# Performance work log

Hardware: AMD Instinct MI355X
Metric: run time of the kernel (lower is better)

Reference implementation:

```python
import jax, jax.numpy as jnp
import numpy as np

NEG_SLOPE = 0.2

def _leaky_relu(x):
    return jnp.where(x >= 0, x, NEG_SLOPE * x)

def setup_inputs() -> dict:
    key = jax.random.key(0)
    ks = jax.random.split(key, 12)
    B, N, M = 64, 4096, 128
    d_ope, d_ma, d_out = 6, 3, 8
    return {
        "ope_ma_adj": jax.random.randint(ks[0], (B, N, M), 0, 2, dtype=jnp.int32),
        "batch_idxes": jnp.arange(B, dtype=jnp.int32),
        "ope_feat": jax.random.normal(ks[1], (B, N, d_ope), dtype=jnp.float32),
        "ma_feat": jax.random.normal(ks[2], (B, M, d_ma), dtype=jnp.float32),
        "proc_time": jax.random.uniform(ks[3], (B, N, M), dtype=jnp.float32),
        "W_src": jax.random.normal(ks[4], (d_ope, d_out), dtype=jnp.float32),
        "W_dst": jax.random.normal(ks[5], (d_ma, d_out), dtype=jnp.float32),
        "w_edge": jax.random.normal(ks[6], (d_out,), dtype=jnp.float32),
        "attn_l": jax.random.normal(ks[7], (d_out,), dtype=jnp.float32),
        "attn_r": jax.random.normal(ks[8], (d_out,), dtype=jnp.float32),
        "attn_e": jax.random.normal(ks[9], (d_out,), dtype=jnp.float32),
    }

def reference(ope_ma_adj, batch_idxes, ope_feat, ma_feat, proc_time,
              W_src, W_dst, w_edge, attn_l, attn_r, attn_e):
    # GATedge.forward with num_head=1 (head dim folded away).
    adj_i = ope_ma_adj[batch_idxes]            # [B,N,M] int (0/1)
    adj = adj_i.astype(jnp.float32)
    feat_src = ope_feat @ W_src                # [B,N,d]
    feat_dst = ma_feat @ W_dst                 # [B,M,d]
    el = feat_src @ attn_l                     # [B,N]
    er = feat_dst @ attn_r                     # [B,M]
    # fc_edge is Linear(1,d): feat_edge = proc[...,None]*w_edge, so
    # ee = (feat_edge*attn_e).sum(-1) = proc * dot(w_edge, attn_e)
    ee = proc_time * jnp.dot(w_edge, attn_e)   # [B,N,M]
    a = adj * el[:, :, None] + ee + adj * er[:, None, :]
    eijk = _leaky_relu(a)                      # [B,N,M]
    ekk = _leaky_relu(2.0 * er)                # [B,M]
    neg_inf = jnp.asarray(-jnp.inf, dtype=eijk.dtype)
    eijk_m = jnp.where(adj_i == 1, eijk, neg_inf)
    e = jnp.concatenate([eijk_m, ekk[:, None, :]], axis=1)   # [B,N+1,M]
    alpha = jax.nn.softmax(e, axis=1)          # softmax over ops (+self)
    alpha_ijk = alpha[:, :-1, :]               # [B,N,M]
    alpha_kk = alpha[:, -1, :]                 # [B,M]
    # b = sum_j alpha_ijk * (feat_edge + feat_src), split to avoid [B,N,M,d]
    b_edge = jnp.einsum('bnm,bnm->bm', alpha_ijk, proc_time)[..., None] * w_edge  # [B,M,d]
    b_src = jnp.einsum('bnm,bnd->bmd', alpha_ijk, feat_src)                       # [B,M,d]
    c = feat_dst * alpha_kk[..., None]         # [B,M,d]
    return jax.nn.sigmoid(b_edge + b_src + c)  # nu_k_prime [B,M,d]
```

## Files before the change

kernel.cpp:

```cpp
#include <hip/hip_runtime.h>
#include <hip/hip_bf16.h>

constexpr int B  = 64;
constexpr int N  = 4096;
constexpr int M  = 128;
constexpr int DO = 8;
constexpr int NC = 32;
constexpr int CH = N / NC;
constexpr int RW = CH / 4;
constexpr int NS = RW / 2;
constexpr float CEXP = 20.0f;

constexpr int waitimm(int n) { return (n & 15) | ((n >> 4) << 14) | (7 << 4) | (15 << 8); }

typedef __attribute__((address_space(3))) void       lds_void;
typedef const __attribute__((address_space(1))) void gbl_void;

__global__ __launch_bounds__(256) void hgnn_k1(
    const int*   __restrict__ adj,
    const int*   __restrict__ bidx,
    const float* __restrict__ ope_feat,
    const float* __restrict__ ma_feat,
    const float* __restrict__ proc,
    const float* __restrict__ W_src,
    const float* __restrict__ W_dst,
    const float* __restrict__ w_edge,
    const float* __restrict__ attn_l,
    const float* __restrict__ attn_r,
    const float* __restrict__ attn_e,
    float*       __restrict__ acc)
{
    const int chunk = blockIdx.x;
    const int b     = blockIdx.y;
    const int t     = threadIdx.x;
    const int w     = t >> 6;
    const int lane  = t & 63;
    const int n0    = chunk * CH;

    __shared__ __align__(16) int   bufA[4][4][256];
    __shared__ __align__(16) float bufP[4][4][256];
    __shared__ __align__(16) float fs[CH][DO];
    __shared__ float el_s[CH];

    const int c0 = lane;
    const int c1 = lane + 64;

    float er0 = 0.f, er1 = 0.f, cee = 0.f;
    {
        const float* mf0 = ma_feat + ((size_t)b * M + c0) * 3;
        const float* mf1 = ma_feat + ((size_t)b * M + c1) * 3;
        const float a0 = mf0[0], a1 = mf0[1], a2 = mf0[2];
        const float b0 = mf1[0], b1 = mf1[1], b2 = mf1[2];
#pragma unroll
        for (int d = 0; d < DO; ++d) {
            er0 += (a0 * W_dst[d] + a1 * W_dst[DO + d] + a2 * W_dst[2 * DO + d]) * attn_r[d];
            er1 += (b0 * W_dst[d] + b1 * W_dst[DO + d] + b2 * W_dst[2 * DO + d]) * attn_r[d];
            cee += w_edge[d] * attn_e[d];
        }
    }

    if (t < CH) {
        const float* of = ope_feat + ((size_t)b * N + (n0 + t)) * 6;
        const float o0 = of[0], o1 = of[1], o2 = of[2], o3 = of[3], o4 = of[4], o5 = of[5];
        float el = 0.f;
#pragma unroll
        for (int d = 0; d < DO; ++d) {
            const float f = o0 * W_src[d] + o1 * W_src[DO + d] + o2 * W_src[2 * DO + d] +
                            o3 * W_src[3 * DO + d] + o4 * W_src[4 * DO + d] + o5 * W_src[5 * DO + d];
            fs[t][d] = f;
            el += f * attn_l[d];
        }
        el_s[t] = el;
    }
    __syncthreads();

    const int ab = bidx[b];
    const int*   adjw  = adj  + ((size_t)ab * N + n0 + w * RW) * M;
    const float* procw = proc + ((size_t)b  * N + n0 + w * RW) * M;
    const int l4 = lane * 4;

    auto issue = [&](int S) {
        __builtin_amdgcn_global_load_lds((gbl_void*)(adjw + (size_t)S * 256 + l4),
                                         (lds_void*)&bufA[w][S & 3][0], 16, 0, 0);
        __builtin_amdgcn_global_load_lds((gbl_void*)(procw + (size_t)S * 256 + l4),
                                         (lds_void*)&bufP[w][S & 3][0], 16, 0, 0);
    };

    float l0 = 0.f, sp0 = 0.f, l1 = 0.f, sp1 = 0.f;
    float sf0[DO], sf1[DO];
#pragma unroll
    for (int d = 0; d < DO; ++d) { sf0[d] = 0.f; sf1[d] = 0.f; }

    auto consume = [&](int S) {
        const int sb = (S & 3) * 256;
        const int* bA = &bufA[w][0][0];
        const float* bP = &bufP[w][0][0];
#pragma unroll
        for (int rr = 0; rr < 2; ++rr) {
            const int r = w * RW + S * 2 + rr;
            const float  el = el_s[r];
            const float4 f0 = *reinterpret_cast<const float4*>(&fs[r][0]);
            const float4 f1 = *reinterpret_cast<const float4*>(&fs[r][4]);
            const int   a0 = bA[sb + rr * 128 + c0];
            const int   a1 = bA[sb + rr * 128 + c1];
            const float p0 = bP[sb + rr * 128 + c0];
            const float p1 = bP[sb + rr * 128 + c1];
            {
                float v = el + er0 + cee * p0;
                v = (v >= 0.f) ? v : 0.2f * v;
                const float wt = __expf(((a0 != 0) ? v : -1e30f) - CEXP);
                l0 += wt; sp0 = fmaf(wt, p0, sp0);
                sf0[0] = fmaf(wt, f0.x, sf0[0]); sf0[1] = fmaf(wt, f0.y, sf0[1]);
                sf0[2] = fmaf(wt, f0.z, sf0[2]); sf0[3] = fmaf(wt, f0.w, sf0[3]);
                sf0[4] = fmaf(wt, f1.x, sf0[4]); sf0[5] = fmaf(wt, f1.y, sf0[5]);
                sf0[6] = fmaf(wt, f1.z, sf0[6]); sf0[7] = fmaf(wt, f1.w, sf0[7]);
            }
            {
                float v = el + er1 + cee * p1;
                v = (v >= 0.f) ? v : 0.2f * v;
                const float wt = __expf(((a1 != 0) ? v : -1e30f) - CEXP);
                l1 += wt; sp1 = fmaf(wt, p1, sp1);
                sf1[0] = fmaf(wt, f0.x, sf1[0]); sf1[1] = fmaf(wt, f0.y, sf1[1]);
                sf1[2] = fmaf(wt, f0.z, sf1[2]); sf1[3] = fmaf(wt, f0.w, sf1[3]);
                sf1[4] = fmaf(wt, f1.x, sf1[4]); sf1[5] = fmaf(wt, f1.y, sf1[5]);
                sf1[6] = fmaf(wt, f1.z, sf1[6]); sf1[7] = fmaf(wt, f1.w, sf1[7]);
            }
        }
    };

    issue(0); issue(1); issue(2); issue(3);

#define STEP_MI(S) { __builtin_amdgcn_s_waitcnt(waitimm(6)); consume(S); issue((S) + 4); }
#define STEP_NI(S, WN) { __builtin_amdgcn_s_waitcnt(waitimm(WN)); consume(S); }
    STEP_MI(0)  STEP_MI(1)  STEP_MI(2)  STEP_MI(3)
    STEP_MI(4)  STEP_MI(5)  STEP_MI(6)  STEP_MI(7)
    STEP_MI(8)  STEP_MI(9)  STEP_MI(10) STEP_MI(11)
    STEP_NI(12, 6) STEP_NI(13, 4) STEP_NI(14, 2) STEP_NI(15, 0)
#undef STEP_MI
#undef STEP_NI

    float* R = reinterpret_cast<float*>(&bufA[0][0][0]);
    const size_t colbase = (size_t)b * M;

    __syncthreads();
    {
        float v0[5] = {l0, sp0, sf0[0], sf0[1], sf0[2]};
        float v1[5] = {l1, sp1, sf1[0], sf1[1], sf1[2]};
#pragma unroll
        for (int k = 0; k < 5; ++k) {
            R[(w * 5 + k) * 128 + c0] = v0[k];
            R[(w * 5 + k) * 128 + c1] = v1[k];
        }
    }
    __syncthreads();
    if (t < M) {
#pragma unroll
        for (int k = 0; k < 5; ++k) {
            const float s = R[(0 * 5 + k) * 128 + t] + R[(1 * 5 + k) * 128 + t] +
                            R[(2 * 5 + k) * 128 + t] + R[(3 * 5 + k) * 128 + t];
            atomicAdd(&acc[(size_t)k * (B * M) + colbase + t], s);
        }
    }
    __syncthreads();
    {
        float v0[5] = {sf0[3], sf0[4], sf0[5], sf0[6], sf0[7]};
        float v1[5] = {sf1[3], sf1[4], sf1[5], sf1[6], sf1[7]};
#pragma unroll
        for (int k = 0; k < 5; ++k) {
            R[(w * 5 + k) * 128 + c0] = v0[k];
            R[(w * 5 + k) * 128 + c1] = v1[k];
        }
    }
    __syncthreads();
    if (t < M) {
#pragma unroll
        for (int k = 0; k < 5; ++k) {
            const float s = R[(0 * 5 + k) * 128 + t] + R[(1 * 5 + k) * 128 + t] +
                            R[(2 * 5 + k) * 128 + t] + R[(3 * 5 + k) * 128 + t];
            atomicAdd(&acc[(size_t)(5 + k) * (B * M) + colbase + t], s);
        }
    }
}

__global__ __launch_bounds__(256) void hgnn_k2(
    const float* __restrict__ ma_feat,
    const float* __restrict__ W_dst,
    const float* __restrict__ w_edge,
    const float* __restrict__ attn_r,
    const float* __restrict__ acc,
    float*       __restrict__ out)
{
    const int t = blockIdx.x * 256 + threadIdx.x;
    if (t >= B * M) return;
    const int m = t & (M - 1);
    const int b = t >> 7;

    float a[10];
#pragma unroll
    for (int f = 0; f < 10; ++f) a[f] = acc[(size_t)f * (B * M) + t];

    const float* mf = ma_feat + ((size_t)b * M + m) * 3;
    const float f0 = mf[0], f1 = mf[1], f2 = mf[2];
    float fd[DO];
    float er = 0.f;
#pragma unroll
    for (int d = 0; d < DO; ++d) {
        fd[d] = f0 * W_dst[d] + f1 * W_dst[DO + d] + f2 * W_dst[2 * DO + d];
        er += fd[d] * attn_r[d];
    }
    float ekk = 2.f * er;
    ekk = (ekk >= 0.f) ? ekk : 0.2f * ekk;
    const float wkk = __expf(ekk - CEXP);

    const float L    = a[0] + wkk;
    const float invL = 1.f / L;
    const float akk  = wkk * invL;
    const float spf  = a[1] * invL;

#pragma unroll
    for (int d = 0; d < DO; ++d) {
        const float x = spf * w_edge[d] + a[2 + d] * invL + fd[d] * akk;
        out[(size_t)t * DO + d] = 1.f / (1.f + __expf(-x));
    }
}

extern "C" void kernel_launch(void* const* d_in, const int* in_sizes, int n_in,
                              void* d_out, int out_size, void* d_ws, size_t ws_size,
                              hipStream_t stream) {
    const int*   adj      = (const int*)  d_in[0];
    const int*   bidx     = (const int*)  d_in[1];
    const float* ope_feat = (const float*)d_in[2];
    const float* ma_feat  = (const float*)d_in[3];
    const float* proc     = (const float*)d_in[4];
    const float* W_src    = (const float*)d_in[5];
    const float* W_dst    = (const float*)d_in[6];
    const float* w_edge   = (const float*)d_in[7];
    const float* attn_l   = (const float*)d_in[8];
    const float* attn_r   = (const float*)d_in[9];
    const float* attn_e   = (const float*)d_in[10];
    float* out = (float*)d_out;
    float* acc = (float*)d_ws;

    hipMemsetAsync(acc, 0, (size_t)10 * B * M * sizeof(float), stream);
    hgnn_k1<<<dim3(NC, B), 256, 0, stream>>>(adj, bidx, ope_feat, ma_feat, proc,
                                             W_src, W_dst, w_edge, attn_l, attn_r,
                                             attn_e, acc);
    hgnn_k2<<<dim3((B * M + 255) / 256), 256, 0, stream>>>(ma_feat, W_dst, w_edge,
                                                           attn_r, acc, out);
}
```

Baseline: 303.3 us.

## Replace LDS-staged async loads with direct register loads and per-thread atomics

Drops the global_load_lds staging buffers and instead loads adj/proc straight into registers with inline-asm dwordx2 loads, using a 4-deep register ring gated by manual vmcnt waits. Each wave now handles interleaved rows (4 waves stride rows) with two adjacent columns per thread. The LDS cross-wave reduction is removed and each thread atomically adds its partials directly, which frees shared memory and lets launch_bounds request 4 blocks per CU. The trade is four times more global atomics per block, and correctness relies on hand-placed waitcnt asm that the compiler does not track.

```diff
diff --git a/kernel.cpp b/kernel.cpp
--- a/kernel.cpp
+++ b/kernel.cpp
@@ -7,16 +7,12 @@
 constexpr int DO = 8;
 constexpr int NC = 32;
 constexpr int CH = N / NC;
-constexpr int RW = CH / 4;
-constexpr int NS = RW / 2;
 constexpr float CEXP = 20.0f;
 
-constexpr int waitimm(int n) { return (n & 15) | ((n >> 4) << 14) | (7 << 4) | (15 << 8); }
-
-typedef __attribute__((address_space(3))) void       lds_void;
-typedef const __attribute__((address_space(1))) void gbl_void;
-
-__global__ __launch_bounds__(256) void hgnn_k1(
+typedef int   v2i __attribute__((ext_vector_type(2)));
+typedef float v2f __attribute__((ext_vector_type(2)));
+
+__global__ __launch_bounds__(256, 4) void hgnn_k1(
     const int*   __restrict__ adj,
     const int*   __restrict__ bidx,
     const float* __restrict__ ope_feat,
@@ -33,17 +29,14 @@
     const int chunk = blockIdx.x;
     const int b     = blockIdx.y;
     const int t     = threadIdx.x;
-    const int w     = t >> 6;
-    const int lane  = t & 63;
+    const int sub   = t >> 6;
+    const int mq    = t & 63;
+    const int c0    = 2 * mq;
+    const int c1    = 2 * mq + 1;
     const int n0    = chunk * CH;
 
-    __shared__ __align__(16) int   bufA[4][4][256];
-    __shared__ __align__(16) float bufP[4][4][256];
     __shared__ __align__(16) float fs[CH][DO];
     __shared__ float el_s[CH];
-
-    const int c0 = lane;
-    const int c1 = lane + 64;
 
     float er0 = 0.f, er1 = 0.f, cee = 0.f;
     {
@@ -75,110 +68,77 @@
     __syncthreads();
 
     const int ab = bidx[b];
-    const int*   adjw  = adj  + ((size_t)ab * N + n0 + w * RW) * M;
-    const float* procw = proc + ((size_t)b  * N + n0 + w * RW) * M;
-    const int l4 = lane * 4;
-
-    auto issue = [&](int S) {
-        __builtin_amdgcn_global_load_lds((gbl_void*)(adjw + (size_t)S * 256 + l4),
-                                         (lds_void*)&bufA[w][S & 3][0], 16, 0, 0);
-        __builtin_amdgcn_global_load_lds((gbl_void*)(procw + (size_t)S * 256 + l4),
-                                         (lds_void*)&bufP[w][S & 3][0], 16, 0, 0);
-    };
+    const int*   gA = adj  + ((size_t)ab * N + n0 + sub) * M + c0;
+    const float* gP = proc + ((size_t)b  * N + n0 + sub) * M + c0;
 
     float l0 = 0.f, sp0 = 0.f, l1 = 0.f, sp1 = 0.f;
     float sf0[DO], sf1[DO];
 #pragma unroll
     for (int d = 0; d < DO; ++d) { sf0[d] = 0.f; sf1[d] = 0.f; }
 
-    auto consume = [&](int S) {
-        const int sb = (S & 3) * 256;
-        const int* bA = &bufA[w][0][0];
-        const float* bP = &bufP[w][0][0];
-#pragma unroll
-        for (int rr = 0; rr < 2; ++rr) {
-            const int r = w * RW + S * 2 + rr;
-            const float  el = el_s[r];
-            const float4 f0 = *reinterpret_cast<const float4*>(&fs[r][0]);
-            const float4 f1 = *reinterpret_cast<const float4*>(&fs[r][4]);
-            const int   a0 = bA[sb + rr * 128 + c0];
-            const int   a1 = bA[sb + rr * 128 + c1];
-            const float p0 = bP[sb + rr * 128 + c0];
-            const float p1 = bP[sb + rr * 128 + c1];
-            {
-                float v = el + er0 + cee * p0;
-                v = (v >= 0.f) ? v : 0.2f * v;
-                const float wt = __expf(((a0 != 0) ? v : -1e30f) - CEXP);
-                l0 += wt; sp0 = fmaf(wt, p0, sp0);
-                sf0[0] = fmaf(wt, f0.x, sf0[0]); sf0[1] = fmaf(wt, f0.y, sf0[1]);
-                sf0[2] = fmaf(wt, f0.z, sf0[2]); sf0[3] = fmaf(wt, f0.w, sf0[3]);
-                sf0[4] = fmaf(wt, f1.x, sf0[4]); sf0[5] = fmaf(wt, f1.y, sf0[5]);
-                sf0[6] = fmaf(wt, f1.z, sf0[6]); sf0[7] = fmaf(wt, f1.w, sf0[7]);
-            }
-            {
-                float v = el + er1 + cee * p1;
-                v = (v >= 0.f) ? v : 0.2f * v;
-                const float wt = __expf(((a1 != 0) ? v : -1e30f) - CEXP);
-                l1 += wt; sp1 = fmaf(wt, p1, sp1);
-                sf1[0] = fmaf(wt, f0.x, sf1[0]); sf1[1] = fmaf(wt, f0.y, sf1[1]);
-                sf1[2] = fmaf(wt, f0.z, sf1[2]); sf1[3] = fmaf(wt, f0.w, sf1[3]);
-                sf1[4] = fmaf(wt, f1.x, sf1[4]); sf1[5] = fmaf(wt, f1.y, sf1[5]);
-                sf1[6] = fmaf(wt, f1.z, sf1[6]); sf1[7] = fmaf(wt, f1.w, sf1[7]);
-            }
+    v2i A[4];
+    v2f P[4];
+
+    auto consume = [&](int j, v2i a, v2f p) {
+        const int r = 4 * j + sub;
+        const float  el = el_s[r];
+        const float4 f0 = *reinterpret_cast<const float4*>(&fs[r][0]);
+        const float4 f1 = *reinterpret_cast<const float4*>(&fs[r][4]);
+        {
+            float v = fmaf(cee, p[0], el + er0);
+            v = fmaxf(v, 0.2f * v);
+            const float wt = __expf(((a[0] != 0) ? v : -1e30f) - CEXP);
+            l0 += wt; sp0 = fmaf(wt, p[0], sp0);
+            sf0[0] = fmaf(wt, f0.x, sf0[0]); sf0[1] = fmaf(wt, f0.y, sf0[1]);
+            sf0[2] = fmaf(wt, f0.z, sf0[2]); sf0[3] = fmaf(wt, f0.w, sf0[3]);
+            sf0[4] = fmaf(wt, f1.x, sf0[4]); sf0[5] = fmaf(wt, f1.y, sf0[5]);
+            sf0[6] = fmaf(wt, f1.z, sf0[6]); sf0[7] = fmaf(wt, f1.w, sf0[7]);
+        }
+        {
+            float v = fmaf(cee, p[1], el + er1);
+            v = fmaxf(v, 0.2f * v);
+            const float wt = __expf(((a[1] != 0) ? v : -1e30f) - CEXP);
+            l1 += wt; sp1 = fmaf(wt, p[1], sp1);
+            sf1[0] = fmaf(wt, f0.x, sf1[0]); sf1[1] = fmaf(wt, f0.y, sf1[1]);
+            sf1[2] = fmaf(wt, f0.z, sf1[2]); sf1[3] = fmaf(wt, f0.w, sf1[3]);
+            sf1[4] = fmaf(wt, f1.x, sf1[4]); sf1[5] = fmaf(wt, f1.y, sf1[5]);
+            sf1[6] = fmaf(wt, f1.z, sf1[6]); sf1[7] = fmaf(wt, f1.w, sf1[7]);
         }
     };
 
-    issue(0); issue(1); issue(2); issue(3);
-
-#define STEP_MI(S) { __builtin_amdgcn_s_waitcnt(waitimm(6)); consume(S); issue((S) + 4); }
-#define STEP_NI(S, WN) { __builtin_amdgcn_s_waitcnt(waitimm(WN)); consume(S); }
-    STEP_MI(0)  STEP_MI(1)  STEP_MI(2)  STEP_MI(3)
-    STEP_MI(4)  STEP_MI(5)  STEP_MI(6)  STEP_MI(7)
-    STEP_MI(8)  STEP_MI(9)  STEP_MI(10) STEP_MI(11)
-    STEP_NI(12, 6) STEP_NI(13, 4) STEP_NI(14, 2) STEP_NI(15, 0)
-#undef STEP_MI
-#undef STEP_NI
-
-    float* R = reinterpret_cast<float*>(&bufA[0][0][0]);
-    const size_t colbase = (size_t)b * M;
-
-    __syncthreads();
-    {
-        float v0[5] = {l0, sp0, sf0[0], sf0[1], sf0[2]};
-        float v1[5] = {l1, sp1, sf1[0], sf1[1], sf1[2]};
-#pragma unroll
-        for (int k = 0; k < 5; ++k) {
-            R[(w * 5 + k) * 128 + c0] = v0[k];
-            R[(w * 5 + k) * 128 + c1] = v1[k];
-        }
-    }
-    __syncthreads();
-    if (t < M) {
-#pragma unroll
-        for (int k = 0; k < 5; ++k) {
-            const float s = R[(0 * 5 + k) * 128 + t] + R[(1 * 5 + k) * 128 + t] +
-                            R[(2 * 5 + k) * 128 + t] + R[(3 * 5 + k) * 128 + t];
-            atomicAdd(&acc[(size_t)k * (B * M) + colbase + t], s);
-        }
-    }
-    __syncthreads();
-    {
-        float v0[5] = {sf0[3], sf0[4], sf0[5], sf0[6], sf0[7]};
-        float v1[5] = {sf1[3], sf1[4], sf1[5], sf1[6], sf1[7]};
-#pragma unroll
-        for (int k = 0; k < 5; ++k) {
-            R[(w * 5 + k) * 128 + c0] = v0[k];
-            R[(w * 5 + k) * 128 + c1] = v1[k];
-        }
-    }
-    __syncthreads();
-    if (t < M) {
-#pragma unroll
-        for (int k = 0; k < 5; ++k) {
-            const float s = R[(0 * 5 + k) * 128 + t] + R[(1 * 5 + k) * 128 + t] +
-                            R[(2 * 5 + k) * 128 + t] + R[(3 * 5 + k) * 128 + t];
-            atomicAdd(&acc[(size_t)(5 + k) * (B * M) + colbase + t], s);
-        }
+#define ISSUE(J)                                                                   \
+    asm volatile("global_load_dwordx2 %0, %1, off"                                 \
+                 : "=v"(A[(J) & 3]) : "v"(gA + (size_t)(J) * 4 * M));              \
+    asm volatile("global_load_dwordx2 %0, %1, off"                                 \
+                 : "=v"(P[(J) & 3]) : "v"(gP + (size_t)(J) * 4 * M));
+
+#define WAITC(J, NSTR)                                                             \
+    asm volatile("s_waitcnt vmcnt(" NSTR ")" : "+v"(A[(J) & 3]), "+v"(P[(J) & 3]));
+
+#define STEP(J)  { WAITC(J, "6") consume(J, A[(J) & 3], P[(J) & 3]); ISSUE((J) + 4) }
+#define TSTEP(J, NSTR) { WAITC(J, NSTR) consume(J, A[(J) & 3], P[(J) & 3]); }
+
+    ISSUE(0) ISSUE(1) ISSUE(2) ISSUE(3)
+    STEP(0)  STEP(1)  STEP(2)  STEP(3)  STEP(4)  STEP(5)  STEP(6)
+    STEP(7)  STEP(8)  STEP(9)  STEP(10) STEP(11) STEP(12) STEP(13)
+    STEP(14) STEP(15) STEP(16) STEP(17) STEP(18) STEP(19) STEP(20)
+    STEP(21) STEP(22) STEP(23) STEP(24) STEP(25) STEP(26) STEP(27)
+    TSTEP(28, "6") TSTEP(29, "4") TSTEP(30, "2") TSTEP(31, "0")
+
+#undef ISSUE
+#undef WAITC
+#undef STEP
+#undef TSTEP
+
+    const size_t cb = (size_t)b * M;
+    atomicAdd(&acc[0 * (size_t)(B * M) + cb + c0], l0);
+    atomicAdd(&acc[0 * (size_t)(B * M) + cb + c1], l1);
+    atomicAdd(&acc[1 * (size_t)(B * M) + cb + c0], sp0);
+    atomicAdd(&acc[1 * (size_t)(B * M) + cb + c1], sp1);
+#pragma unroll
+    for (int d = 0; d < DO; ++d) {
+        atomicAdd(&acc[(size_t)(2 + d) * (B * M) + cb + c0], sf0[d]);
+        atomicAdd(&acc[(size_t)(2 + d) * (B * M) + cb + c1], sf1[d]);
     }
 }
 
```

Result: slower. 461.8 us (+52.3%).
